# Performance work log

Hardware: AMD Instinct MI355X
Metric: run time of the kernel (lower is better)

The kernel has to match this reference:

```python
import math
import jax, jax.numpy as jnp
import numpy as np

CAPACITY_FACTOR = 1.0
MIN_CAPACITY = 8


def setup_inputs() -> dict:
    key = jax.random.key(0)
    k1, k2 = jax.random.split(key)
    s, d, e = 8192, 1024, 64
    inputs = jax.random.normal(k1, (s, d), dtype=jnp.float32)
    wg_weight = jax.random.normal(k2, (e, d), dtype=jnp.float32) * (1.0 / math.sqrt(d))
    return {"inputs": inputs, "wg_weight": wg_weight}


def reference(inputs, wg_weight):
    # gate projection (always fp32 in the original)
    logits = inputs.astype(jnp.float32) @ wg_weight.T  # [s, e]
    s, e = logits.shape
    # static capacity: ceil(s/e * capacity_factor), floored at min_capacity
    capacity = max(int(math.ceil(s / e * CAPACITY_FACTOR)), MIN_CAPACITY)

    gates = jax.nn.softmax(logits, axis=1)            # [s, e]
    indices = jnp.argmax(gates, axis=1)               # [s]
    mask = jax.nn.one_hot(indices, e, dtype=jnp.int32)  # [s, e]
    exp_counts = jnp.sum(mask, axis=0)                # [e]

    # load-balancing aux loss (uses mask BEFORE capacity dropping)
    me = jnp.mean(gates, axis=0)
    ce = jnp.mean(mask.astype(jnp.float32), axis=0)
    l_aux = jnp.sum(me * ce) * e

    # capacity dropping: with use_rts=False, topk over the binary mask keeps
    # the first `capacity` tokens routed to each expert, i.e. cumulative
    # position-in-expert < capacity
    positions = jnp.cumsum(mask, axis=0) - 1          # [s, e]
    mask = mask * (positions < capacity).astype(jnp.int32)

    locations = jnp.cumsum(mask, axis=0) - 1          # [s, e]
    locations_s = jnp.sum(locations * mask, axis=1)   # [s] slot per token

    gates = gates * mask.astype(jnp.float32)          # zero out dropped tokens
    locations_sc = jax.nn.one_hot(locations_s, capacity, dtype=jnp.float32)  # [s, c]
    combine_weights = jnp.einsum('se,sc->sec', gates, locations_sc)  # [s, e, c]
    dispatch_mask = combine_weights.astype(bool)
    return l_aux, combine_weights, dispatch_mask, exp_counts
```

## Files before the change

kernel.cpp:

```cpp
#include <hip/hip_runtime.h>
#include <cstdint>
#include <cstddef>

#define S 8192
#define Dm 1024
#define E 64
#define CAP 128
#define SEC 67108864ull

#define GEMM_BLOCKS 256
#define FILL_BLOCKS 1792
#define N4ALL 33554448u

typedef float f32x4 __attribute__((ext_vector_type(4)));

__global__ __launch_bounds__(256) void k_main(const float* __restrict__ x,
                                              const float* __restrict__ w,
                                              float* __restrict__ gate,
                                              int* __restrict__ idx,
                                              float* __restrict__ me_part,
                                              float* __restrict__ out) {
    int bid = blockIdx.x;
    int tid = threadIdx.x;
    if (bid < GEMM_BLOCKS) {
        __shared__ float Al[2][32][68];
        __shared__ float Wl[2][64][68];
        __shared__ float sm[32];
        __shared__ float sinv[32];
        int rt = (tid & 15) * 2;
        int ce = (tid >> 4) * 4;
        int t0 = bid * 32;
        const float* asrc = x + (size_t)(t0 + (tid >> 3)) * Dm + (tid & 7) * 8;
        const float* wsrc0 = w + (size_t)(tid >> 3) * Dm + (tid & 7) * 8;
        const float* wsrc1 = wsrc0 + 32 * (size_t)Dm;
        int sr = tid >> 3;
        int sc = (tid & 7) * 8;

        float4 acc0 = make_float4(0.f, 0.f, 0.f, 0.f);
        float4 acc1 = make_float4(0.f, 0.f, 0.f, 0.f);

        float4 pa0 = *(const float4*)(asrc + 0);
        float4 pa1 = *(const float4*)(asrc + 4);
        float4 pw0 = *(const float4*)(wsrc0 + 0);
        float4 pw1 = *(const float4*)(wsrc0 + 4);
        float4 pw2 = *(const float4*)(wsrc1 + 0);
        float4 pw3 = *(const float4*)(wsrc1 + 4);
        float4 qa0 = *(const float4*)(asrc + 64);
        float4 qa1 = *(const float4*)(asrc + 68);
        float4 qw0 = *(const float4*)(wsrc0 + 64);
        float4 qw1 = *(const float4*)(wsrc0 + 68);
        float4 qw2 = *(const float4*)(wsrc1 + 64);
        float4 qw3 = *(const float4*)(wsrc1 + 68);

#define WRITE_LDS(B, A0, A1, W0, W1, W2, W3)                                   \
        *(float4*)&Al[B][sr][sc] = A0;                                         \
        *(float4*)&Al[B][sr][sc + 4] = A1;                                     \
        *(float4*)&Wl[B][sr][sc] = W0;                                         \
        *(float4*)&Wl[B][sr][sc + 4] = W1;                                     \
        *(float4*)&Wl[B][32 + sr][sc] = W2;                                    \
        *(float4*)&Wl[B][32 + sr][sc + 4] = W3;

#define LOADP(KB)                                                              \
        pa0 = *(const float4*)(asrc + (KB));                                   \
        pa1 = *(const float4*)(asrc + (KB) + 4);                               \
        pw0 = *(const float4*)(wsrc0 + (KB));                                  \
        pw1 = *(const float4*)(wsrc0 + (KB) + 4);                              \
        pw2 = *(const float4*)(wsrc1 + (KB));                                  \
        pw3 = *(const float4*)(wsrc1 + (KB) + 4);

#define LOADQ(KB)                                                              \
        qa0 = *(const float4*)(asrc + (KB));                                   \
        qa1 = *(const float4*)(asrc + (KB) + 4);                               \
        qw0 = *(const float4*)(wsrc0 + (KB));                                  \
        qw1 = *(const float4*)(wsrc0 + (KB) + 4);                              \
        qw2 = *(const float4*)(wsrc1 + (KB));                                  \
        qw3 = *(const float4*)(wsrc1 + (KB) + 4);

#define INNER_COMPUTE(B)                                                       \
        _Pragma("unroll 4")                                                    \
        for (int k4 = 0; k4 < 16; ++k4) {                                      \
            float4 a0 = *(const float4*)&Al[B][rt][k4 * 4];                    \
            float4 a1 = *(const float4*)&Al[B][rt + 1][k4 * 4];                \
            float4 w0 = *(const float4*)&Wl[B][ce + 0][k4 * 4];                \
            float4 w1 = *(const float4*)&Wl[B][ce + 1][k4 * 4];                \
            float4 w2 = *(const float4*)&Wl[B][ce + 2][k4 * 4];                \
            float4 w3 = *(const float4*)&Wl[B][ce + 3][k4 * 4];                \
            acc0.x = fmaf(a0.w, w0.w, fmaf(a0.z, w0.z, fmaf(a0.y, w0.y, fmaf(a0.x, w0.x, acc0.x)))); \
            acc0.y = fmaf(a0.w, w1.w, fmaf(a0.z, w1.z, fmaf(a0.y, w1.y, fmaf(a0.x, w1.x, acc0.y)))); \
            acc0.z = fmaf(a0.w, w2.w, fmaf(a0.z, w2.z, fmaf(a0.y, w2.y, fmaf(a0.x, w2.x, acc0.z)))); \
            acc0.w = fmaf(a0.w, w3.w, fmaf(a0.z, w3.z, fmaf(a0.y, w3.y, fmaf(a0.x, w3.x, acc0.w)))); \
            acc1.x = fmaf(a1.w, w0.w, fmaf(a1.z, w0.z, fmaf(a1.y, w0.y, fmaf(a1.x, w0.x, acc1.x)))); \
            acc1.y = fmaf(a1.w, w1.w, fmaf(a1.z, w1.z, fmaf(a1.y, w1.y, fmaf(a1.x, w1.x, acc1.y)))); \
            acc1.z = fmaf(a1.w, w2.w, fmaf(a1.z, w2.z, fmaf(a1.y, w2.y, fmaf(a1.x, w2.x, acc1.z)))); \
            acc1.w = fmaf(a1.w, w3.w, fmaf(a1.z, w3.z, fmaf(a1.y, w3.y, fmaf(a1.x, w3.x, acc1.w)))); \
        }

        WRITE_LDS(0, pa0, pa1, pw0, pw1, pw2, pw3)
        LOADP(2 * 64)
        __syncthreads();

        for (int ch = 0; ch < 16; ch += 2) {
            WRITE_LDS(1, qa0, qa1, qw0, qw1, qw2, qw3)
            if (ch + 3 < 16) { LOADQ((ch + 3) * 64) }
            INNER_COMPUTE(0)
            __syncthreads();
            if (ch + 2 < 16) { WRITE_LDS(0, pa0, pa1, pw0, pw1, pw2, pw3) }
            if (ch + 4 < 16) { LOADP((ch + 4) * 64) }
            INNER_COMPUTE(1)
            __syncthreads();
        }
#undef WRITE_LDS
#undef LOADP
#undef LOADQ
#undef INNER_COMPUTE
        Al[0][rt][ce + 0] = acc0.x; Al[0][rt][ce + 1] = acc0.y;
        Al[0][rt][ce + 2] = acc0.z; Al[0][rt][ce + 3] = acc0.w;
        Al[0][rt + 1][ce + 0] = acc1.x; Al[0][rt + 1][ce + 1] = acc1.y;
        Al[0][rt + 1][ce + 2] = acc1.z; Al[0][rt + 1][ce + 3] = acc1.w;
        __syncthreads();
        if (tid < 32) {
            float m = Al[0][tid][0];
            int am = 0;
#pragma unroll
            for (int c = 1; c < E; ++c) {
                float v = Al[0][tid][c];
                if (v > m) { m = v; am = c; }
            }
            float ssum = 0.f;
#pragma unroll
            for (int c = 0; c < E; ++c) ssum += __expf(Al[0][tid][c] - m);
            float inv = 1.0f / ssum;
            gate[t0 + tid] = inv;
            idx[t0 + tid] = am;
            sm[tid] = m;
            sinv[tid] = inv;
        }
        __syncthreads();
        if (tid < E) {
            float cs = 0.f;
#pragma unroll 8
            for (int r = 0; r < 32; ++r)
                cs += __expf(Al[0][r][tid] - sm[r]) * sinv[r];
            me_part[bid * E + tid] = cs;
        }
    } else {
        int fb = bid - GEMM_BLOCKS;
        f32x4 z = {0.f, 0.f, 0.f, 0.f};
        f32x4* o4 = (f32x4*)out;
        for (unsigned i = (unsigned)fb * 256u + tid; i < N4ALL;
             i += FILL_BLOCKS * 256u)
            o4[i] = z;
    }
}

__global__ __launch_bounds__(256) void k_scan(const int* __restrict__ idx,
                                              const float* __restrict__ gate,
                                              const float* __restrict__ me_part,
                                              float* __restrict__ out) {
    int e = blockIdx.x;
    int tid = threadIdx.x;
    int lane = tid & 63;
    int wid = tid >> 6;
    __shared__ int wsum[4];
    __shared__ float red[256];
    int running = 0;
    for (int ch = 0; ch < S / 256; ++ch) {
        int t = ch * 256 + tid;
        bool f = (idx[t] == e);
        unsigned long long b = __ballot(f);
        int pre = __popcll(b & ((1ull << lane) - 1ull));
        if (lane == 0) wsum[wid] = __popcll(b);
        __syncthreads();
        int off = running;
#pragma unroll
        for (int w2 = 0; w2 < 4; ++w2)
            if (w2 < wid) off += wsum[w2];
        int p = off + pre;
        if (f && p < CAP) {
            size_t o = 1 + (size_t)t * (E * CAP) + (size_t)e * CAP + (size_t)p;
            out[o] = gate[t];
            out[o + (size_t)SEC] = 1.0f;
        }
        running += wsum[0] + wsum[1] + wsum[2] + wsum[3];
        __syncthreads();
    }
    red[tid] = me_part[tid * E + e];
    __syncthreads();
    for (int s2 = 128; s2 > 0; s2 >>= 1) {
        if (tid < s2) red[tid] += red[tid + s2];
        __syncthreads();
    }
    if (tid == 0) {
        out[1 + 2 * (size_t)SEC + e] = (float)running;
        float la = red[0] * (1.0f / (float)S) *
                   ((float)running / (float)S) * (float)E;
        atomicAdd(out, la);
    }
}

extern "C" void kernel_launch(void* const* d_in, const int* in_sizes, int n_in,
                              void* d_out, int out_size, void* d_ws, size_t ws_size,
                              hipStream_t stream) {
    const float* x = (const float*)d_in[0];
    const float* w = (const float*)d_in[1];
    float* out = (float*)d_out;

    float* me_part = (float*)d_ws;
    float* gate = me_part + GEMM_BLOCKS * E;
    int* idx = (int*)(gate + S);

    k_main<<<dim3(GEMM_BLOCKS + FILL_BLOCKS), dim3(256), 0, stream>>>(
        x, w, gate, idx, me_part, out);
    k_scan<<<dim3(64), dim3(256), 0, stream>>>(idx, gate, me_part, out);
}
```

Before: 138.0 us.

## Compute gate GEMM with split-fp16 MFMA instead of scalar fp32 FMA

Replaces the scalar fp32 FMA inner loop of the gate projection with MFMA 16x16x32 fp16 instructions. Each fp32 operand is split into high and low fp16 parts, and three products (hi*hi, lo*hi, hi*lo) recover near-fp32 accuracy. The weights are pre-scaled by 4096 to avoid fp16 underflow in the low part. LDS double buffering is replaced by a single buffer with extra barriers, and the split conversion adds ALU work per load. The GEMM is small relative to the large output zero-fill, so the gain may be limited.

```diff
diff --git a/kernel.cpp b/kernel.cpp
--- a/kernel.cpp
+++ b/kernel.cpp
@@ -11,8 +11,26 @@
 #define GEMM_BLOCKS 256
 #define FILL_BLOCKS 1792
 #define N4ALL 33554448u
+#define WSCALE 4096.0f
+#define INV_WSCALE (1.0f / 4096.0f)
 
 typedef float f32x4 __attribute__((ext_vector_type(4)));
+typedef _Float16 f16x8 __attribute__((ext_vector_type(8)));
+typedef float f32x4b __attribute__((ext_vector_type(4)));
+
+#define CV8(H, L, ROW, COL, V0, V1, SCALE) do {                                \
+    f16x8 hh, ll; float t_;                                                    \
+    t_ = (V0).x * (SCALE); hh[0] = (_Float16)t_; ll[0] = (_Float16)(t_ - (float)hh[0]); \
+    t_ = (V0).y * (SCALE); hh[1] = (_Float16)t_; ll[1] = (_Float16)(t_ - (float)hh[1]); \
+    t_ = (V0).z * (SCALE); hh[2] = (_Float16)t_; ll[2] = (_Float16)(t_ - (float)hh[2]); \
+    t_ = (V0).w * (SCALE); hh[3] = (_Float16)t_; ll[3] = (_Float16)(t_ - (float)hh[3]); \
+    t_ = (V1).x * (SCALE); hh[4] = (_Float16)t_; ll[4] = (_Float16)(t_ - (float)hh[4]); \
+    t_ = (V1).y * (SCALE); hh[5] = (_Float16)t_; ll[5] = (_Float16)(t_ - (float)hh[5]); \
+    t_ = (V1).z * (SCALE); hh[6] = (_Float16)t_; ll[6] = (_Float16)(t_ - (float)hh[6]); \
+    t_ = (V1).w * (SCALE); hh[7] = (_Float16)t_; ll[7] = (_Float16)(t_ - (float)hh[7]); \
+    *(f16x8*)&H[ROW][COL] = hh;                                                \
+    *(f16x8*)&L[ROW][COL] = ll;                                                \
+} while (0)
 
 __global__ __launch_bounds__(256) void k_main(const float* __restrict__ x,
                                               const float* __restrict__ w,
@@ -23,21 +41,28 @@
     int bid = blockIdx.x;
     int tid = threadIdx.x;
     if (bid < GEMM_BLOCKS) {
-        __shared__ float Al[2][32][68];
-        __shared__ float Wl[2][64][68];
+        __shared__ _Float16 Ah[32][80];
+        __shared__ _Float16 Alo[32][80];
+        __shared__ _Float16 Wh[64][80];
+        __shared__ _Float16 Wlo[64][80];
+        __shared__ float Sl[32][66];
         __shared__ float sm[32];
         __shared__ float sinv[32];
-        int rt = (tid & 15) * 2;
-        int ce = (tid >> 4) * 4;
         int t0 = bid * 32;
-        const float* asrc = x + (size_t)(t0 + (tid >> 3)) * Dm + (tid & 7) * 8;
-        const float* wsrc0 = w + (size_t)(tid >> 3) * Dm + (tid & 7) * 8;
-        const float* wsrc1 = wsrc0 + 32 * (size_t)Dm;
         int sr = tid >> 3;
         int sc = (tid & 7) * 8;
-
-        float4 acc0 = make_float4(0.f, 0.f, 0.f, 0.f);
-        float4 acc1 = make_float4(0.f, 0.f, 0.f, 0.f);
+        const float* asrc = x + (size_t)(t0 + sr) * Dm + (tid & 7) * 8;
+        const float* wsrc0 = w + (size_t)sr * Dm + (tid & 7) * 8;
+        const float* wsrc1 = wsrc0 + 32 * (size_t)Dm;
+
+        int wv = tid >> 6;
+        int l = tid & 63;
+        int lr = l & 15;
+        int lg = l >> 4;
+        int mt = wv & 1;
+        int np = wv >> 1;
+        f32x4b acc0 = {0.f, 0.f, 0.f, 0.f};
+        f32x4b acc1 = {0.f, 0.f, 0.f, 0.f};
 
         float4 pa0 = *(const float4*)(asrc + 0);
         float4 pa1 = *(const float4*)(asrc + 4);
@@ -52,13 +77,10 @@
         float4 qw2 = *(const float4*)(wsrc1 + 64);
         float4 qw3 = *(const float4*)(wsrc1 + 68);
 
-#define WRITE_LDS(B, A0, A1, W0, W1, W2, W3)                                   \
-        *(float4*)&Al[B][sr][sc] = A0;                                         \
-        *(float4*)&Al[B][sr][sc + 4] = A1;                                     \
-        *(float4*)&Wl[B][sr][sc] = W0;                                         \
-        *(float4*)&Wl[B][sr][sc + 4] = W1;                                     \
-        *(float4*)&Wl[B][32 + sr][sc] = W2;                                    \
-        *(float4*)&Wl[B][32 + sr][sc + 4] = W3;
+#define WRITE_LDS(A0, A1, W0, W1, W2, W3)                                      \
+        CV8(Ah, Alo, sr, sc, A0, A1, 1.0f);                                    \
+        CV8(Wh, Wlo, sr, sc, W0, W1, WSCALE);                                  \
+        CV8(Wh, Wlo, (32 + sr), sc, W2, W3, WSCALE);
 
 #define LOADP(KB)                                                              \
         pa0 = *(const float4*)(asrc + (KB));                                   \
@@ -76,59 +98,58 @@
         qw2 = *(const float4*)(wsrc1 + (KB));                                  \
         qw3 = *(const float4*)(wsrc1 + (KB) + 4);
 
-#define INNER_COMPUTE(B)                                                       \
-        _Pragma("unroll 4")                                                    \
-        for (int k4 = 0; k4 < 16; ++k4) {                                      \
-            float4 a0 = *(const float4*)&Al[B][rt][k4 * 4];                    \
-            float4 a1 = *(const float4*)&Al[B][rt + 1][k4 * 4];                \
-            float4 w0 = *(const float4*)&Wl[B][ce + 0][k4 * 4];                \
-            float4 w1 = *(const float4*)&Wl[B][ce + 1][k4 * 4];                \
-            float4 w2 = *(const float4*)&Wl[B][ce + 2][k4 * 4];                \
-            float4 w3 = *(const float4*)&Wl[B][ce + 3][k4 * 4];                \
-            acc0.x = fmaf(a0.w, w0.w, fmaf(a0.z, w0.z, fmaf(a0.y, w0.y, fmaf(a0.x, w0.x, acc0.x)))); \
-            acc0.y = fmaf(a0.w, w1.w, fmaf(a0.z, w1.z, fmaf(a0.y, w1.y, fmaf(a0.x, w1.x, acc0.y)))); \
-            acc0.z = fmaf(a0.w, w2.w, fmaf(a0.z, w2.z, fmaf(a0.y, w2.y, fmaf(a0.x, w2.x, acc0.z)))); \
-            acc0.w = fmaf(a0.w, w3.w, fmaf(a0.z, w3.z, fmaf(a0.y, w3.y, fmaf(a0.x, w3.x, acc0.w)))); \
-            acc1.x = fmaf(a1.w, w0.w, fmaf(a1.z, w0.z, fmaf(a1.y, w0.y, fmaf(a1.x, w0.x, acc1.x)))); \
-            acc1.y = fmaf(a1.w, w1.w, fmaf(a1.z, w1.z, fmaf(a1.y, w1.y, fmaf(a1.x, w1.x, acc1.y)))); \
-            acc1.z = fmaf(a1.w, w2.w, fmaf(a1.z, w2.z, fmaf(a1.y, w2.y, fmaf(a1.x, w2.x, acc1.z)))); \
-            acc1.w = fmaf(a1.w, w3.w, fmaf(a1.z, w3.z, fmaf(a1.y, w3.y, fmaf(a1.x, w3.x, acc1.w)))); \
-        }
-
-        WRITE_LDS(0, pa0, pa1, pw0, pw1, pw2, pw3)
-        LOADP(2 * 64)
-        __syncthreads();
+#define INNER_MFMA                                                             \
+        _Pragma("unroll")                                                      \
+        for (int ks = 0; ks < 2; ++ks) {                                       \
+            int kc = ks * 32 + lg * 8;                                         \
+            f16x8 ah = *(const f16x8*)&Ah[mt * 16 + lr][kc];                   \
+            f16x8 al = *(const f16x8*)&Alo[mt * 16 + lr][kc];                  \
+            f16x8 bh0 = *(const f16x8*)&Wh[np * 32 + lr][kc];                  \
+            f16x8 bl0 = *(const f16x8*)&Wlo[np * 32 + lr][kc];                 \
+            f16x8 bh1 = *(const f16x8*)&Wh[np * 32 + 16 + lr][kc];             \
+            f16x8 bl1 = *(const f16x8*)&Wlo[np * 32 + 16 + lr][kc];            \
+            acc0 = __builtin_amdgcn_mfma_f32_16x16x32_f16(ah, bh0, acc0, 0, 0, 0); \
+            acc0 = __builtin_amdgcn_mfma_f32_16x16x32_f16(al, bh0, acc0, 0, 0, 0); \
+            acc0 = __builtin_amdgcn_mfma_f32_16x16x32_f16(ah, bl0, acc0, 0, 0, 0); \
+            acc1 = __builtin_amdgcn_mfma_f32_16x16x32_f16(ah, bh1, acc1, 0, 0, 0); \
+            acc1 = __builtin_amdgcn_mfma_f32_16x16x32_f16(al, bh1, acc1, 0, 0, 0); \
+            acc1 = __builtin_amdgcn_mfma_f32_16x16x32_f16(ah, bl1, acc1, 0, 0, 0); \
+        }
 
         for (int ch = 0; ch < 16; ch += 2) {
-            WRITE_LDS(1, qa0, qa1, qw0, qw1, qw2, qw3)
+            __syncthreads();
+            WRITE_LDS(pa0, pa1, pw0, pw1, pw2, pw3)
+            __syncthreads();
+            if (ch + 2 < 16) { LOADP((ch + 2) * 64) }
+            INNER_MFMA
+            __syncthreads();
+            WRITE_LDS(qa0, qa1, qw0, qw1, qw2, qw3)
+            __syncthreads();
             if (ch + 3 < 16) { LOADQ((ch + 3) * 64) }
-            INNER_COMPUTE(0)
-            __syncthreads();
-            if (ch + 2 < 16) { WRITE_LDS(0, pa0, pa1, pw0, pw1, pw2, pw3) }
-            if (ch + 4 < 16) { LOADP((ch + 4) * 64) }
-            INNER_COMPUTE(1)
-            __syncthreads();
+            INNER_MFMA
         }
 #undef WRITE_LDS
 #undef LOADP
 #undef LOADQ
-#undef INNER_COMPUTE
-        Al[0][rt][ce + 0] = acc0.x; Al[0][rt][ce + 1] = acc0.y;
-        Al[0][rt][ce + 2] = acc0.z; Al[0][rt][ce + 3] = acc0.w;
-        Al[0][rt + 1][ce + 0] = acc1.x; Al[0][rt + 1][ce + 1] = acc1.y;
-        Al[0][rt + 1][ce + 2] = acc1.z; Al[0][rt + 1][ce + 3] = acc1.w;
+#undef INNER_MFMA
+        __syncthreads();
+#pragma unroll
+        for (int r = 0; r < 4; ++r) {
+            Sl[mt * 16 + lg * 4 + r][np * 32 + lr] = acc0[r] * INV_WSCALE;
+            Sl[mt * 16 + lg * 4 + r][np * 32 + 16 + lr] = acc1[r] * INV_WSCALE;
+        }
         __syncthreads();
         if (tid < 32) {
-            float m = Al[0][tid][0];
+            float m = Sl[tid][0];
             int am = 0;
 #pragma unroll
             for (int c = 1; c < E; ++c) {
-                float v = Al[0][tid][c];
+                float v = Sl[tid][c];
                 if (v > m) { m = v; am = c; }
             }
             float ssum = 0.f;
 #pragma unroll
-            for (int c = 0; c < E; ++c) ssum += __expf(Al[0][tid][c] - m);
+            for (int c = 0; c < E; ++c) ssum += __expf(Sl[tid][c] - m);
             float inv = 1.0f / ssum;
             gate[t0 + tid] = inv;
             idx[t0 + tid] = am;
@@ -140,7 +161,7 @@
             float cs = 0.f;
 #pragma unroll 8
             for (int r = 0; r < 32; ++r)
-                cs += __expf(Al[0][r][tid] - sm[r]) * sinv[r];
+                cs += __expf(Sl[r][tid] - sm[r]) * sinv[r];
             me_part[bid * E + tid] = cs;
         }
     } else {
```

Result: no change. 136.7 us (-1.0%).
